# Kernel optimization log

Hardware: AMD Instinct MI355X
Metric: run time of the kernel (lower is better)

The kernel has to match this reference:

```python
import jax, jax.numpy as jnp
import numpy as np

HIDDEN = 512
EXP = 2048  # hidden * expansion_factor(4)

def _glorot(key, shape):
    fan_in = shape[0]
    return jax.random.normal(key, shape, dtype=jnp.float32) / np.sqrt(fan_in)

def setup_inputs() -> dict:
    key = jax.random.key(0)
    ks = jax.random.split(key, 6)
    B, S = 4, 4096
    return {
        "x": jax.random.normal(ks[0], (B, S, HIDDEN), dtype=jnp.float32),
        "W_in1": _glorot(ks[1], (HIDDEN, EXP)),
        "b_in1": jnp.zeros((EXP,), jnp.float32),
        "W_in2": _glorot(ks[2], (HIDDEN, EXP)),
        "b_in2": jnp.zeros((EXP,), jnp.float32),
        "W_z": _glorot(ks[3], (EXP, EXP)),
        "b_z": jnp.zeros((EXP,), jnp.float32),
        "W_h": _glorot(ks[4], (EXP, EXP)),
        "b_h": jnp.zeros((EXP,), jnp.float32),
        "W_out": _glorot(ks[5], (EXP, HIDDEN)),
        "b_out": jnp.zeros((HIDDEN,), jnp.float32),
    }

def _min_gru(x_in, W_z, b_z, W_h, b_h):
    # minGRU: h_t = (1 - z_t) * h_{t-1} + z_t * h_tilde_t, h_0 = 0
    z = jax.nn.sigmoid(jnp.einsum("bse,ef->bsf", x_in, W_z) + b_z)
    h_tilde = jnp.einsum("bse,ef->bsf", x_in, W_h) + b_h
    a = 1.0 - z          # decay coeff
    b = z * h_tilde      # input term
    def combine(c1, c2):
        a1, b1 = c1
        a2, b2 = c2
        return (a1 * a2, b1 * a2 + b2)
    _, h = jax.lax.associative_scan(combine, (a, b), axis=1)
    return h

def reference(x, W_in1, b_in1, W_in2, b_in2, W_z, b_z, W_h, b_h, W_out, b_out):
    x_in = jax.nn.silu(jnp.einsum("bsd,de->bse", x, W_in1) + b_in1)
    x_skip = jax.nn.silu(jnp.einsum("bsd,de->bse", x, W_in2) + b_in2)
    h = _min_gru(x_in, W_z, b_z, W_h, b_h)
    return jnp.einsum("bse,ed->bsd", x_skip + h, W_out) + b_out
```

## Files before the change

kernel.cpp:

```cpp
#include <hip/hip_runtime.h>
#include <hip/hip_bf16.h>


typedef __bf16 bf16x8 __attribute__((ext_vector_type(8)));
typedef __bf16 bf16x4 __attribute__((ext_vector_type(4)));
typedef float  f32x4  __attribute__((ext_vector_type(4)));

#define DEVINL __device__ __forceinline__

DEVINL void async_ld16(const __bf16* g, __bf16* l) {
    __builtin_amdgcn_global_load_lds(
        (const __attribute__((address_space(1))) void*)g,
        (__attribute__((address_space(3))) void*)l, 16, 0, 0);
}

DEVINL float fsigmoid(float v) { return 1.0f / (1.0f + __expf(-v)); }

template <int MODE>
__global__ __launch_bounds__(512, 2)
void gemm3(const __bf16* __restrict__ A, const __bf16* __restrict__ Bt,
           const float* __restrict__ bias, const float* __restrict__ bias2,
           void* __restrict__ out, void* __restrict__ out2, int N, int K,
           int bps, int seg_stride, int row_off)
{
    __shared__ union SM3 {
        __bf16 kl[4][2][256 * 32];
        __bf16 ct[64 * 264];
    } sm;
    const int tid = threadIdx.x;
    const int bx = blockIdx.x;
    const int seg = bx / bps;
    const int within = bx - seg * bps;
    const int gm0 = row_off + seg * seg_stride + within * 256;
    const int om0 = bx * 256;
    const int n0 = blockIdx.y * 256;

    const int c0 = tid, c1 = tid + 512;
    const int r0 = c0 >> 2, k0 = (c0 & 3) ^ ((c0 >> 3) & 3);
    const int r1 = c1 >> 2, k1 = (c1 & 3) ^ ((c1 >> 3) & 3);
    const __bf16* Ag0 = A  + (size_t)(gm0 + r0) * K + k0 * 8;
    const __bf16* Ag1 = A  + (size_t)(gm0 + r1) * K + k1 * 8;
    const __bf16* Bg0 = Bt + (size_t)(n0 + r0) * K + k0 * 8;
    const __bf16* Bg1 = Bt + (size_t)(n0 + r1) * K + k1 * 8;

    const int lane = tid & 63;
    const int wave = tid >> 6;
    const int wm = wave >> 2;
    const int wn = wave & 3;
    const int quad = lane >> 4;
    const int r = lane & 15;
    const int swz = (quad ^ ((r >> 1) & 3)) * 8;

    f32x4 acc[8][4] = {};

    const int T = K >> 5;

    auto stage = [&](int t, int b) {
        const int kt = t << 5;
        async_ld16(Ag0 + kt, sm.kl[b][0] + c0 * 8);
        async_ld16(Ag1 + kt, sm.kl[b][0] + c1 * 8);
        async_ld16(Bg0 + kt, sm.kl[b][1] + c0 * 8);
        async_ld16(Bg1 + kt, sm.kl[b][1] + c1 * 8);
    };

    stage(0, 0);
    stage(1, 1);
    stage(2, 2);

    for (int t = 0; t < T; ++t) {
        if (t + 2 < T) {
            asm volatile("s_waitcnt vmcnt(8)\n\ts_barrier" ::: "memory");
        } else if (t + 1 < T) {
            asm volatile("s_waitcnt vmcnt(4)\n\ts_barrier" ::: "memory");
        } else {
            asm volatile("s_waitcnt vmcnt(0)\n\ts_barrier" ::: "memory");
        }
        if (t + 3 < T) stage(t + 3, (t + 3) & 3);

        const __bf16* ap = sm.kl[t & 3][0] + (wm * 128 + r) * 32 + swz;
        const __bf16* bp = sm.kl[t & 3][1] + (wn * 64 + r) * 32 + swz;
        bf16x8 af[8], bf_[4];
#pragma unroll
        for (int m = 0; m < 8; ++m) af[m] = *(const bf16x8*)(ap + m * 512);
#pragma unroll
        for (int n = 0; n < 4; ++n) bf_[n] = *(const bf16x8*)(bp + n * 512);

        __builtin_amdgcn_s_setprio(1);
#pragma unroll
        for (int m = 0; m < 8; ++m)
#pragma unroll
            for (int n = 0; n < 4; ++n)
                acc[m][n] = __builtin_amdgcn_mfma_f32_16x16x32_bf16(
                    af[m], bf_[n], acc[m][n], 0, 0, 0);
        __builtin_amdgcn_s_setprio(0);
    }

    __syncthreads();

    const bool lo = n0 < 2048;
    __bf16* dst;
    int cb;
    size_t stride;
    if (MODE == 0) {
        dst = lo ? (__bf16*)out : (__bf16*)out2;
        cb = lo ? n0 : n0 - 2048;
        stride = 2048;
    } else {
        dst = (__bf16*)out;
        cb = n0;
        stride = (size_t)N;
    }
    float bvj[4];
#pragma unroll
    for (int nf = 0; nf < 4; ++nf) {
        const int gc = n0 + wn * 64 + nf * 16 + r;
        bvj[nf] = lo ? bias[gc] : bias2[gc - 2048];
    }

#pragma unroll
    for (int p = 0; p < 4; ++p) {
        if (wm == (p >> 1)) {
            const int mb = (p & 1) * 4;
#pragma unroll
            for (int mm = 0; mm < 4; ++mm)
#pragma unroll
                for (int nf = 0; nf < 4; ++nf)
#pragma unroll
                    for (int k = 0; k < 4; ++k) {
                        const float v = acc[mb + mm][nf][k] + bvj[nf];
                        const __bf16 o = (MODE == 0) ? (__bf16)(v * fsigmoid(v))
                                                     : (__bf16)v;
                        sm.ct[(mm * 16 + quad * 4 + k) * 264 +
                              (wn * 64 + nf * 16 + r)] = o;
                    }
        }
        __syncthreads();
#pragma unroll
        for (int q = 0; q < 4; ++q) {
            const int chunk = q * 512 + tid;
            const int trow = chunk >> 5;
            const int tc = (chunk & 31) * 8;
            const bf16x8 vv = *(const bf16x8*)(sm.ct + trow * 264 + tc);
            *(bf16x8*)(dst + (size_t)(om0 + p * 64 + trow) * stride + cb + tc) = vv;
        }
        __syncthreads();
    }
}

struct KLoopSM { __bf16 A[2][128 * 32]; __bf16 B[2][128 * 32]; };

template <int MODE>
__global__ __launch_bounds__(256)
void gemm_bt(const __bf16* __restrict__ A, const __bf16* __restrict__ Bt,
             const float* __restrict__ bias, const float* __restrict__ bias2,
             void* __restrict__ out, void* __restrict__ out2, int N, int K,
             int bps, int seg_stride, int row_off)
{
    __shared__ union SM {
        KLoopSM kl;
        __bf16 ct[64 * 136];
        float  ctf[32 * 132];
    } sm;
    const int tid = threadIdx.x;
    const int bx = blockIdx.x;
    const int seg = bx / bps;
    const int within = bx - seg * bps;
    const int gm0 = row_off + seg * seg_stride + within * 128;
    const int om0 = bx * 128;
    const int n0 = blockIdx.y * 128;

    const int c0 = tid, c1 = tid + 256;
    const int r0 = c0 >> 2, k0 = (c0 & 3) ^ ((c0 >> 3) & 3);
    const int r1 = c1 >> 2, k1 = (c1 & 3) ^ ((c1 >> 3) & 3);
    const __bf16* Ag0 = A  + (size_t)(gm0 + r0) * K + k0 * 8;
    const __bf16* Ag1 = A  + (size_t)(gm0 + r1) * K + k1 * 8;
    const __bf16* Bg0 = Bt + (size_t)(n0 + r0) * K + k0 * 8;
    const __bf16* Bg1 = Bt + (size_t)(n0 + r1) * K + k1 * 8;

    const int lane = tid & 63;
    const int wave = tid >> 6;
    const int wrow = (wave >> 1) * 64;
    const int wcol = (wave & 1) * 64;
    const int quad = lane >> 4;
    const int r = lane & 15;
    const int swz = (quad ^ ((r >> 1) & 3)) * 8;

    f32x4 acc[4][4] = {};

    const int T = K >> 5;
    async_ld16(Ag0, sm.kl.A[0] + c0 * 8);
    async_ld16(Ag1, sm.kl.A[0] + c1 * 8);
    async_ld16(Bg0, sm.kl.B[0] + c0 * 8);
    async_ld16(Bg1, sm.kl.B[0] + c1 * 8);

    for (int t = 0; t < T; ++t) {
        const int cur = t & 1;
        if (t + 1 < T) {
            const int kt = (t + 1) << 5;
            async_ld16(Ag0 + kt, sm.kl.A[cur ^ 1] + c0 * 8);
            async_ld16(Ag1 + kt, sm.kl.A[cur ^ 1] + c1 * 8);
            async_ld16(Bg0 + kt, sm.kl.B[cur ^ 1] + c0 * 8);
            async_ld16(Bg1 + kt, sm.kl.B[cur ^ 1] + c1 * 8);
            asm volatile("s_waitcnt vmcnt(4)\n\ts_barrier" ::: "memory");
        } else {
            asm volatile("s_waitcnt vmcnt(0)\n\ts_barrier" ::: "memory");
        }

        const __bf16* ap = sm.kl.A[cur] + (wrow + r) * 32 + swz;
        const __bf16* bp = sm.kl.B[cur] + (wcol + r) * 32 + swz;
        bf16x8 af[4], bf_[4];
#pragma unroll
        for (int i = 0; i < 4; ++i) af[i] = *(const bf16x8*)(ap + i * 512);
#pragma unroll
        for (int i = 0; i < 4; ++i) bf_[i] = *(const bf16x8*)(bp + i * 512);
#pragma unroll
        for (int i = 0; i < 4; ++i)
#pragma unroll
            for (int j = 0; j < 4; ++j)
                acc[i][j] = __builtin_amdgcn_mfma_f32_16x16x32_bf16(
                    af[i], bf_[j], acc[i][j], 0, 0, 0);

        asm volatile("s_waitcnt lgkmcnt(0)\n\ts_barrier" ::: "memory");
    }

    if (MODE == 3) {
        float bvj[4];
#pragma unroll
        for (int j = 0; j < 4; ++j)
            bvj[j] = bias[n0 + wcol + j * 16 + r];
#pragma unroll
        for (int p = 0; p < 4; ++p) {
#pragma unroll
            for (int j = 0; j < 4; ++j)
#pragma unroll
                for (int k = 0; k < 4; ++k)
                    sm.ctf[((wave >> 1) * 16 + quad * 4 + k) * 132 +
                           (wcol + j * 16 + r)] = acc[p][j][k] + bvj[j];
            __syncthreads();
#pragma unroll
            for (int q = 0; q < 4; ++q) {
                const int chunk = q * 256 + tid;
                const int trow = chunk >> 5;
                const int tc4 = (chunk & 31) * 4;
                const f32x4 vv = *(const f32x4*)(sm.ctf + trow * 132 + tc4);
                const int grow = om0 + (trow >> 4) * 64 + p * 16 + (trow & 15);
                *(f32x4*)((float*)out + (size_t)grow * N + n0 + tc4) = vv;
            }
            __syncthreads();
        }
    } else {
        const bool lo = n0 < 2048;
        __bf16* dst;
        int cb;
        size_t stride;
        if (MODE == 0) {
            dst = lo ? (__bf16*)out : (__bf16*)out2;
            cb = lo ? n0 : n0 - 2048;
            stride = 2048;
        } else {
            dst = (__bf16*)out;
            cb = n0;
            stride = (size_t)N;
        }
        float bvj[4];
#pragma unroll
        for (int j = 0; j < 4; ++j) {
            const int gc = n0 + wcol + j * 16 + r;
            bvj[j] = lo ? bias[gc] : bias2[gc - 2048];
        }
#pragma unroll
        for (int p = 0; p < 2; ++p) {
#pragma unroll
            for (int ii = 0; ii < 2; ++ii) {
                const int i = 2 * p + ii;
#pragma unroll
                for (int j = 0; j < 4; ++j)
#pragma unroll
                    for (int k = 0; k < 4; ++k) {
                        const float v = acc[i][j][k] + bvj[j];
                        const __bf16 o = (MODE == 0) ? (__bf16)(v * fsigmoid(v))
                                                     : (__bf16)v;
                        sm.ct[((wave >> 1) * 32 + ii * 16 + quad * 4 + k) * 136 +
                              (wcol + j * 16 + r)] = o;
                    }
            }
            __syncthreads();
#pragma unroll
            for (int q = 0; q < 4; ++q) {
                const int chunk = q * 256 + tid;
                const int trow = chunk >> 4;
                const int tc = (chunk & 15) * 8;
                const bf16x8 vv = *(const bf16x8*)(sm.ct + trow * 136 + tc);
                const int grow = om0 + (trow >> 5) * 64 + p * 32 + (trow & 31);
                *(bf16x8*)(dst + (size_t)grow * stride + cb + tc) = vv;
            }
            __syncthreads();
        }
    }
}

#define SSEG 32
#define SCOLS 32
__global__ __launch_bounds__(1024)
void scan_kernel(const __bf16* __restrict__ raw, __bf16* __restrict__ xskip,
                 float* __restrict__ carry, int CS, int S, int t0, int first)
{
    __shared__ float Als[SSEG][SCOLS];
    __shared__ float Bls[SSEG][SCOLS];
    const int lane = threadIdx.x & (SCOLS - 1);
    const int w = threadIdx.x >> 5;
    const int nb8 = gridDim.x >> 3;
    const int lin = (blockIdx.x & 7) * nb8 + (blockIdx.x >> 3);
    const int gpb = 2048 / SCOLS;
    const int batch = lin / gpb;
    const int col = (lin - batch * gpb) * SCOLS + lane;
    const int L = CS / SSEG;
    const int tbeg = w * L;

    const size_t rbase = ((size_t)batch * CS + tbeg) * 4096 + col;

    float av[32], bv[32];
    float A = 1.0f, Bv = 0.0f;
    {
        size_t idx = rbase;
#pragma unroll
        for (int t = 0; t < 32; ++t, idx += 4096) {
            const float z = fsigmoid((float)raw[idx]);
            const float b = z * (float)raw[idx + 2048];
            const float a = 1.0f - z;
            av[t] = a;
            bv[t] = b;
            Bv = a * Bv + b;
            A *= a;
        }
    }
    Als[w][lane] = A;
    Bls[w][lane] = Bv;
    __syncthreads();

    const int ch = batch * 2048 + col;
    float h = first ? 0.0f : carry[ch];
    for (int s = 0; s < w; ++s)
        h = Als[s][lane] * h + Bls[s][lane];
    if (w == SSEG - 1)
        carry[ch] = A * h + Bv;

    {
        size_t gidx = ((size_t)batch * S + t0 + tbeg) * 2048 + col;
#pragma unroll
        for (int t = 0; t < 32; ++t, gidx += 2048) {
            h = av[t] * h + bv[t];
            xskip[gidx] = (__bf16)((float)xskip[gidx] + h);
        }
    }
}

__global__ __launch_bounds__(256)
void conv_f32_bf16(const float* __restrict__ x, __bf16* __restrict__ y, int n4)
{
    const int i = blockIdx.x * 256 + threadIdx.x;
    if (i >= n4) return;
    const float4 v = ((const float4*)x)[i];
    bf16x4 o;
    o[0] = (__bf16)v.x; o[1] = (__bf16)v.y; o[2] = (__bf16)v.z; o[3] = (__bf16)v.w;
    ((bf16x4*)y)[i] = o;
}

__global__ __launch_bounds__(256)
void transpose_bf16(const float* __restrict__ W, __bf16* __restrict__ Wt, int K, int N)
{
    __shared__ float tile[32][33];
    const int tx = threadIdx.x & 31;
    const int ty = threadIdx.x >> 5;
    const int nb = blockIdx.x * 32;
    const int kb = blockIdx.y * 32;
#pragma unroll
    for (int i = 0; i < 32; i += 8)
        tile[ty + i][tx] = W[(size_t)(kb + ty + i) * N + nb + tx];
    __syncthreads();
#pragma unroll
    for (int i = 0; i < 32; i += 8)
        Wt[(size_t)(nb + ty + i) * K + kb + tx] = (__bf16)tile[tx][ty + i];
}

extern "C" void kernel_launch(void* const* d_in, const int* in_sizes, int n_in,
                              void* d_out, int out_size, void* d_ws, size_t ws_size,
                              hipStream_t stream)
{
    const float* x     = (const float*)d_in[0];
    const float* W_in1 = (const float*)d_in[1];
    const float* b_in1 = (const float*)d_in[2];
    const float* W_in2 = (const float*)d_in[3];
    const float* b_in2 = (const float*)d_in[4];
    const float* W_z   = (const float*)d_in[5];
    const float* b_z   = (const float*)d_in[6];
    const float* W_h   = (const float*)d_in[7];
    const float* b_h   = (const float*)d_in[8];
    const float* W_out = (const float*)d_in[9];
    const float* b_out = (const float*)d_in[10];

    const int B = 4, S = 4096, H = 512, E = 2048;
    const int M = B * S;
    const int CS = 1024;
    const int NC = S / CS;
    const int MC = B * CS;

    const size_t MiB = 1024 * 1024;
    const size_t NEEDED = 183 * MiB;
    if (ws_size < NEEDED) return;

    char* ws = (char*)d_ws;
    __bf16* xb    = (__bf16*)(ws + 0);
    __bf16* rawzh = (__bf16*)(ws + 0);
    float*  carry = (float*) (ws + 32 * MiB);
    __bf16* xin   = (__bf16*)(ws + 33 * MiB);
    __bf16* xskip = (__bf16*)(ws + 97 * MiB);
    __bf16* Wt12  = (__bf16*)(ws + 161 * MiB);
    __bf16* Wtzh  = (__bf16*)(ws + 165 * MiB);
    __bf16* Wto   = (__bf16*)(ws + 181 * MiB);

    conv_f32_bf16<<<(M * H / 4 + 255) / 256, 256, 0, stream>>>(x, xb, M * H / 4);
    transpose_bf16<<<dim3(E / 32, H / 32), 256, 0, stream>>>(W_in1, Wt12, H, E);
    transpose_bf16<<<dim3(E / 32, H / 32), 256, 0, stream>>>(W_in2, Wt12 + (size_t)E * H, H, E);
    transpose_bf16<<<dim3(E / 32, E / 32), 256, 0, stream>>>(W_z, Wtzh, E, E);
    transpose_bf16<<<dim3(E / 32, E / 32), 256, 0, stream>>>(W_h, Wtzh + (size_t)E * E, E, E);
    transpose_bf16<<<dim3(H / 32, E / 32), 256, 0, stream>>>(W_out, Wto, E, H);

    gemm3<0><<<dim3(M / 256, 2 * E / 256), 512, 0, stream>>>(
        xb, Wt12, b_in1, b_in2, xin, xskip, 2 * E, H, M / 256, 0, 0);

    for (int c = 0; c < NC; ++c) {
        const int row_off = c * CS;
        gemm3<4><<<dim3(MC / 256, 2 * E / 256), 512, 0, stream>>>(
            xin, Wtzh, b_z, b_h, rawzh, nullptr, 2 * E, E, CS / 256, S, row_off);
        scan_kernel<<<(B * E) / SCOLS, 1024, 0, stream>>>(
            rawzh, xskip, carry, CS, S, row_off, c == 0);
    }

    gemm_bt<3><<<dim3(M / 128, H / 128), 256, 0, stream>>>(
        xskip, Wto, b_out, nullptr, (float*)d_out, nullptr, H, E, M / 128, 0, 0);
}
```

Before: 607.2 us.

## Interleave async tile loads with MFMA phases in gemm3; use gemm_bt for input projection

The gemm3 main loop is split into four phases. Each phase loads two A fragments, issues one of the four async global-to-LDS loads for the next stage, and runs a slice of the MFMA work, with s_barriers between phases so load issue and compute interleave across waves. The input projection GEMM (K=512) now uses the smaller 128x128 gemm_bt kernel instead of the 256x256 gemm3, giving more blocks for the short K loop. The extra barriers add sync cost per K step, and the A fragments are now loaded in pairs instead of all at once.

```diff
diff --git a/kernel.cpp b/kernel.cpp
--- a/kernel.cpp
+++ b/kernel.cpp
@@ -75,24 +75,72 @@
         } else {
             asm volatile("s_waitcnt vmcnt(0)\n\ts_barrier" ::: "memory");
         }
-        if (t + 3 < T) stage(t + 3, (t + 3) & 3);
+
+        const bool st = (t + 3) < T;
+        const int sb = (t + 3) & 3;
+        const int skt = (t + 3) << 5;
 
         const __bf16* ap = sm.kl[t & 3][0] + (wm * 128 + r) * 32 + swz;
         const __bf16* bp = sm.kl[t & 3][1] + (wn * 64 + r) * 32 + swz;
-        bf16x8 af[8], bf_[4];
-#pragma unroll
-        for (int m = 0; m < 8; ++m) af[m] = *(const bf16x8*)(ap + m * 512);
+
+        bf16x8 bf_[4];
 #pragma unroll
         for (int n = 0; n < 4; ++n) bf_[n] = *(const bf16x8*)(bp + n * 512);
-
-        __builtin_amdgcn_s_setprio(1);
-#pragma unroll
-        for (int m = 0; m < 8; ++m)
-#pragma unroll
-            for (int n = 0; n < 4; ++n)
-                acc[m][n] = __builtin_amdgcn_mfma_f32_16x16x32_bf16(
-                    af[m], bf_[n], acc[m][n], 0, 0, 0);
-        __builtin_amdgcn_s_setprio(0);
+        {
+            bf16x8 a0 = *(const bf16x8*)(ap + 0 * 512);
+            bf16x8 a1 = *(const bf16x8*)(ap + 1 * 512);
+            if (st) async_ld16(Ag0 + skt, sm.kl[sb][0] + c0 * 8);
+            asm volatile("s_barrier" ::: "memory");
+            __builtin_amdgcn_s_setprio(1);
+#pragma unroll
+            for (int n = 0; n < 4; ++n) {
+                acc[0][n] = __builtin_amdgcn_mfma_f32_16x16x32_bf16(a0, bf_[n], acc[0][n], 0, 0, 0);
+                acc[1][n] = __builtin_amdgcn_mfma_f32_16x16x32_bf16(a1, bf_[n], acc[1][n], 0, 0, 0);
+            }
+            __builtin_amdgcn_s_setprio(0);
+            asm volatile("s_barrier" ::: "memory");
+        }
+        {
+            bf16x8 a0 = *(const bf16x8*)(ap + 2 * 512);
+            bf16x8 a1 = *(const bf16x8*)(ap + 3 * 512);
+            if (st) async_ld16(Ag1 + skt, sm.kl[sb][0] + c1 * 8);
+            asm volatile("s_barrier" ::: "memory");
+            __builtin_amdgcn_s_setprio(1);
+#pragma unroll
+            for (int n = 0; n < 4; ++n) {
+                acc[2][n] = __builtin_amdgcn_mfma_f32_16x16x32_bf16(a0, bf_[n], acc[2][n], 0, 0, 0);
+                acc[3][n] = __builtin_amdgcn_mfma_f32_16x16x32_bf16(a1, bf_[n], acc[3][n], 0, 0, 0);
+            }
+            __builtin_amdgcn_s_setprio(0);
+            asm volatile("s_barrier" ::: "memory");
+        }
+        {
+            bf16x8 a0 = *(const bf16x8*)(ap + 4 * 512);
+            bf16x8 a1 = *(const bf16x8*)(ap + 5 * 512);
+            if (st) async_ld16(Bg0 + skt, sm.kl[sb][1] + c0 * 8);
+            asm volatile("s_barrier" ::: "memory");
+            __builtin_amdgcn_s_setprio(1);
+#pragma unroll
+            for (int n = 0; n < 4; ++n) {
+                acc[4][n] = __builtin_amdgcn_mfma_f32_16x16x32_bf16(a0, bf_[n], acc[4][n], 0, 0, 0);
+                acc[5][n] = __builtin_amdgcn_mfma_f32_16x16x32_bf16(a1, bf_[n], acc[5][n], 0, 0, 0);
+            }
+            __builtin_amdgcn_s_setprio(0);
+            asm volatile("s_barrier" ::: "memory");
+        }
+        {
+            bf16x8 a0 = *(const bf16x8*)(ap + 6 * 512);
+            bf16x8 a1 = *(const bf16x8*)(ap + 7 * 512);
+            if (st) async_ld16(Bg1 + skt, sm.kl[sb][1] + c1 * 8);
+            asm volatile("s_barrier" ::: "memory");
+            __builtin_amdgcn_s_setprio(1);
+#pragma unroll
+            for (int n = 0; n < 4; ++n) {
+                acc[6][n] = __builtin_amdgcn_mfma_f32_16x16x32_bf16(a0, bf_[n], acc[6][n], 0, 0, 0);
+                acc[7][n] = __builtin_amdgcn_mfma_f32_16x16x32_bf16(a1, bf_[n], acc[7][n], 0, 0, 0);
+            }
+            __builtin_amdgcn_s_setprio(0);
+        }
     }
 
     __syncthreads();
@@ -163,11 +211,12 @@
     } sm;
     const int tid = threadIdx.x;
     const int bx = blockIdx.x;
+    const int by = blockIdx.y;
     const int seg = bx / bps;
     const int within = bx - seg * bps;
     const int gm0 = row_off + seg * seg_stride + within * 128;
     const int om0 = bx * 128;
-    const int n0 = blockIdx.y * 128;
+    const int n0 = by * 128;
 
     const int c0 = tid, c1 = tid + 256;
     const int r0 = c0 >> 2, k0 = (c0 & 3) ^ ((c0 >> 3) & 3);
@@ -426,8 +475,8 @@
     transpose_bf16<<<dim3(E / 32, E / 32), 256, 0, stream>>>(W_h, Wtzh + (size_t)E * E, E, E);
     transpose_bf16<<<dim3(H / 32, E / 32), 256, 0, stream>>>(W_out, Wto, E, H);
 
-    gemm3<0><<<dim3(M / 256, 2 * E / 256), 512, 0, stream>>>(
-        xb, Wt12, b_in1, b_in2, xin, xskip, 2 * E, H, M / 256, 0, 0);
+    gemm_bt<0><<<dim3(M / 128, 2 * E / 128), 256, 0, stream>>>(
+        xb, Wt12, b_in1, b_in2, xin, xskip, 2 * E, H, M / 128, 0, 0);
 
     for (int c = 0; c < NC; ++c) {
         const int row_off = c * CS;
```

New measurement: 620.9 us. +2.2%, slower.

## Shrink z/h GEMM tile to 128x256 with double buffering and higher occupancy

Applied to the files above, without the earlier changes.

Replaces the 256x256 four-stage pipelined gemm3 with gemm4, which uses a 128x256 tile, two LDS buffers, half the accumulators and launch bounds targeting four blocks per CU. It also moves the input projection GEMM back to the 128x128 gemm_bt kernel. The goal is more resident waves and more blocks for the chunked z/h GEMM, trading away per-tile reuse and the deeper prefetch pipeline. The extra barrier each iteration and the shallower prefetch could expose more memory latency.

```diff
diff --git a/kernel.cpp b/kernel.cpp
--- a/kernel.cpp
+++ b/kernel.cpp
@@ -17,31 +17,32 @@
 DEVINL float fsigmoid(float v) { return 1.0f / (1.0f + __expf(-v)); }
 
 template <int MODE>
-__global__ __launch_bounds__(512, 2)
-void gemm3(const __bf16* __restrict__ A, const __bf16* __restrict__ Bt,
+__global__ __launch_bounds__(512, 4)
+void gemm4(const __bf16* __restrict__ A, const __bf16* __restrict__ Bt,
            const float* __restrict__ bias, const float* __restrict__ bias2,
            void* __restrict__ out, void* __restrict__ out2, int N, int K,
            int bps, int seg_stride, int row_off)
 {
-    __shared__ union SM3 {
-        __bf16 kl[4][2][256 * 32];
+    struct KL { __bf16 A[128 * 32]; __bf16 B[256 * 32]; };
+    __shared__ union SM4 {
+        KL kl[2];
         __bf16 ct[64 * 264];
     } sm;
     const int tid = threadIdx.x;
     const int bx = blockIdx.x;
     const int seg = bx / bps;
     const int within = bx - seg * bps;
-    const int gm0 = row_off + seg * seg_stride + within * 256;
-    const int om0 = bx * 256;
+    const int gm0 = row_off + seg * seg_stride + within * 128;
+    const int om0 = bx * 128;
     const int n0 = blockIdx.y * 256;
 
+    const int rA = tid >> 2,         kA = (tid & 3) ^ ((tid >> 3) & 3);
     const int c0 = tid, c1 = tid + 512;
-    const int r0 = c0 >> 2, k0 = (c0 & 3) ^ ((c0 >> 3) & 3);
-    const int r1 = c1 >> 2, k1 = (c1 & 3) ^ ((c1 >> 3) & 3);
-    const __bf16* Ag0 = A  + (size_t)(gm0 + r0) * K + k0 * 8;
-    const __bf16* Ag1 = A  + (size_t)(gm0 + r1) * K + k1 * 8;
-    const __bf16* Bg0 = Bt + (size_t)(n0 + r0) * K + k0 * 8;
-    const __bf16* Bg1 = Bt + (size_t)(n0 + r1) * K + k1 * 8;
+    const int rB0 = c0 >> 2,         kB0 = (c0 & 3) ^ ((c0 >> 3) & 3);
+    const int rB1 = c1 >> 2,         kB1 = (c1 & 3) ^ ((c1 >> 3) & 3);
+    const __bf16* Ag  = A  + (size_t)(gm0 + rA)  * K + kA  * 8;
+    const __bf16* Bg0 = Bt + (size_t)(n0 + rB0) * K + kB0 * 8;
+    const __bf16* Bg1 = Bt + (size_t)(n0 + rB1) * K + kB1 * 8;
 
     const int lane = tid & 63;
     const int wave = tid >> 6;
@@ -51,65 +52,52 @@
     const int r = lane & 15;
     const int swz = (quad ^ ((r >> 1) & 3)) * 8;
 
-    f32x4 acc[8][4] = {};
+    f32x4 acc[4][4] = {};
 
     const int T = K >> 5;
 
     auto stage = [&](int t, int b) {
         const int kt = t << 5;
-        async_ld16(Ag0 + kt, sm.kl[b][0] + c0 * 8);
-        async_ld16(Ag1 + kt, sm.kl[b][0] + c1 * 8);
-        async_ld16(Bg0 + kt, sm.kl[b][1] + c0 * 8);
-        async_ld16(Bg1 + kt, sm.kl[b][1] + c1 * 8);
+        async_ld16(Ag  + kt, sm.kl[b].A + tid * 8);
+        async_ld16(Bg0 + kt, sm.kl[b].B + c0 * 8);
+        async_ld16(Bg1 + kt, sm.kl[b].B + c1 * 8);
     };
 
     stage(0, 0);
-    stage(1, 1);
-    stage(2, 2);
 
     for (int t = 0; t < T; ++t) {
-        if (t + 2 < T) {
-            asm volatile("s_waitcnt vmcnt(8)\n\ts_barrier" ::: "memory");
-        } else if (t + 1 < T) {
-            asm volatile("s_waitcnt vmcnt(4)\n\ts_barrier" ::: "memory");
+        const int cur = t & 1;
+        if (t + 1 < T) {
+            stage(t + 1, cur ^ 1);
+            asm volatile("s_waitcnt vmcnt(3)\n\ts_barrier" ::: "memory");
         } else {
             asm volatile("s_waitcnt vmcnt(0)\n\ts_barrier" ::: "memory");
         }
-        if (t + 3 < T) stage(t + 3, (t + 3) & 3);
-
-        const __bf16* ap = sm.kl[t & 3][0] + (wm * 128 + r) * 32 + swz;
-        const __bf16* bp = sm.kl[t & 3][1] + (wn * 64 + r) * 32 + swz;
-        bf16x8 af[8], bf_[4];
-#pragma unroll
-        for (int m = 0; m < 8; ++m) af[m] = *(const bf16x8*)(ap + m * 512);
+
+        const __bf16* ap = sm.kl[cur].A + (wm * 64 + r) * 32 + swz;
+        const __bf16* bp = sm.kl[cur].B + (wn * 64 + r) * 32 + swz;
+        bf16x8 af[4], bf_[4];
+#pragma unroll
+        for (int m = 0; m < 4; ++m) af[m] = *(const bf16x8*)(ap + m * 512);
 #pragma unroll
         for (int n = 0; n < 4; ++n) bf_[n] = *(const bf16x8*)(bp + n * 512);
 
         __builtin_amdgcn_s_setprio(1);
 #pragma unroll
-        for (int m = 0; m < 8; ++m)
+        for (int m = 0; m < 4; ++m)
 #pragma unroll
             for (int n = 0; n < 4; ++n)
                 acc[m][n] = __builtin_amdgcn_mfma_f32_16x16x32_bf16(
                     af[m], bf_[n], acc[m][n], 0, 0, 0);
         __builtin_amdgcn_s_setprio(0);
-    }
-
-    __syncthreads();
+
+        asm volatile("s_waitcnt lgkmcnt(0)\n\ts_barrier" ::: "memory");
+    }
 
     const bool lo = n0 < 2048;
-    __bf16* dst;
-    int cb;
-    size_t stride;
-    if (MODE == 0) {
-        dst = lo ? (__bf16*)out : (__bf16*)out2;
-        cb = lo ? n0 : n0 - 2048;
-        stride = 2048;
-    } else {
-        dst = (__bf16*)out;
-        cb = n0;
-        stride = (size_t)N;
-    }
+    __bf16* dst = (__bf16*)out;
+    const int cb = n0;
+    const size_t stride = (size_t)N;
     float bvj[4];
 #pragma unroll
     for (int nf = 0; nf < 4; ++nf) {
@@ -118,20 +106,17 @@
     }
 
 #pragma unroll
-    for (int p = 0; p < 4; ++p) {
-        if (wm == (p >> 1)) {
-            const int mb = (p & 1) * 4;
+    for (int p = 0; p < 2; ++p) {
+        if (wm == p) {
 #pragma unroll
             for (int mm = 0; mm < 4; ++mm)
 #pragma unroll
                 for (int nf = 0; nf < 4; ++nf)
 #pragma unroll
                     for (int k = 0; k < 4; ++k) {
-                        const float v = acc[mb + mm][nf][k] + bvj[nf];
-                        const __bf16 o = (MODE == 0) ? (__bf16)(v * fsigmoid(v))
-                                                     : (__bf16)v;
+                        const float v = acc[mm][nf][k] + bvj[nf];
                         sm.ct[(mm * 16 + quad * 4 + k) * 264 +
-                              (wn * 64 + nf * 16 + r)] = o;
+                              (wn * 64 + nf * 16 + r)] = (__bf16)v;
                     }
         }
         __syncthreads();
@@ -163,11 +148,12 @@
     } sm;
     const int tid = threadIdx.x;
     const int bx = blockIdx.x;
+    const int by = blockIdx.y;
     const int seg = bx / bps;
     const int within = bx - seg * bps;
     const int gm0 = row_off + seg * seg_stride + within * 128;
     const int om0 = bx * 128;
-    const int n0 = blockIdx.y * 128;
+    const int n0 = by * 128;
 
     const int c0 = tid, c1 = tid + 256;
     const int r0 = c0 >> 2, k0 = (c0 & 3) ^ ((c0 >> 3) & 3);
@@ -426,13 +412,13 @@
     transpose_bf16<<<dim3(E / 32, E / 32), 256, 0, stream>>>(W_h, Wtzh + (size_t)E * E, E, E);
     transpose_bf16<<<dim3(H / 32, E / 32), 256, 0, stream>>>(W_out, Wto, E, H);
 
-    gemm3<0><<<dim3(M / 256, 2 * E / 256), 512, 0, stream>>>(
-        xb, Wt12, b_in1, b_in2, xin, xskip, 2 * E, H, M / 256, 0, 0);
+    gemm_bt<0><<<dim3(M / 128, 2 * E / 128), 256, 0, stream>>>(
+        xb, Wt12, b_in1, b_in2, xin, xskip, 2 * E, H, M / 128, 0, 0);
 
     for (int c = 0; c < NC; ++c) {
         const int row_off = c * CS;
-        gemm3<4><<<dim3(MC / 256, 2 * E / 256), 512, 0, stream>>>(
-            xin, Wtzh, b_z, b_h, rawzh, nullptr, 2 * E, E, CS / 256, S, row_off);
+        gemm4<4><<<dim3(MC / 128, 2 * E / 256), 512, 0, stream>>>(
+            xin, Wtzh, b_z, b_h, rawzh, nullptr, 2 * E, E, CS / 128, S, row_off);
         scan_kernel<<<(B * E) / SCOLS, 1024, 0, stream>>>(
             rawzh, xskip, carry, CS, S, row_off, c == 0);
     }
```

New measurement: 652.5 us. +7.5%, slower.
